# Kernel tuning notes

Hardware: AMD Instinct MI355X
Metric: run time of the kernel (lower is better)

Reference implementation:

```python
import jax, jax.numpy as jnp
import numpy as np
import math

B, NMAX, PE, E, DS, NF = 8, 128, 64, 5, 64, 8  # E = num_edge_features + 1


def setup_inputs() -> dict:
    key = jax.random.key(0)
    ks = jax.random.split(key, 10)
    total = B * NMAX
    x = jax.random.normal(ks[0], (total, PE), jnp.float32)
    batch = jnp.arange(total, dtype=jnp.int32) // NMAX  # sorted graph ids, full graphs
    q = jax.random.uniform(ks[1], (B,), jnp.float32, 0.1, 0.9)  # keep sin(2*pi*q) away from 0
    s = 0.05
    return dict(
        x=x, batch=batch, q=q,
        w_attn=jax.random.normal(ks[2], (PE, 4 * E * PE), jnp.float32) * s,
        b_attn=jnp.zeros((4 * E * PE,), jnp.float32),
        w_node=jax.random.normal(ks[3], (PE, NF), jnp.float32) * s,
        b_node=jnp.zeros((NF,), jnp.float32),
        w_phi=jax.random.normal(ks[4], (DS,), jnp.float32) * s,   # Linear(1, DS) weight
        b_phi=jax.random.normal(ks[5], (DS,), jnp.float32) * s,
        w_ctx=jax.random.normal(ks[6], (DS, DS), jnp.float32) * s,  # Linear(DS, DS, bias=False)
        w_self=jax.random.normal(ks[7], (DS,), jnp.float32) * s,  # Linear(1, DS) weight
        b_self=jax.random.normal(ks[8], (DS,), jnp.float32) * s,
        w_out=jax.random.normal(ks[9], (DS,), jnp.float32) * s,   # Linear(DS, 1) weight
        b_out=jnp.zeros((), jnp.float32),
    )


def _to_dense(batch, vals, n_graphs, n_max):
    # torch_geometric.to_dense_batch for sorted batch vector
    starts = jnp.searchsorted(batch, jnp.arange(n_graphs, dtype=batch.dtype))
    pos = jnp.arange(batch.shape[0]) - starts[batch]
    dense = jnp.zeros((n_graphs, n_max, vals.shape[-1]), vals.dtype).at[batch, pos].set(vals)
    mask = jnp.zeros((n_graphs, n_max), bool).at[batch, pos].set(True)
    return dense, mask


def reference(x, batch, q, w_attn, b_attn, w_node, b_node,
              w_phi, b_phi, w_ctx, w_self, b_self, w_out, b_out):
    scale = 1.0 / math.sqrt(E * PE)
    x_hat = x @ w_node + b_node                              # (total, NF)
    proj = x @ w_attn + b_attn                               # (total, 4*E*PE)
    dense, mask = _to_dense(batch, proj, B, NMAX)            # (B, N, 4*E*PE), (B, N)
    k1, q1, k2, q2 = jnp.split(dense, 4, axis=-1)
    heads = lambda t: t.reshape(B, NMAX, E, PE).transpose(0, 2, 1, 3)  # (B, E, N, PE)
    k1, q1, k2, q2 = heads(k1), heads(q1), heads(k2), heads(q2)
    z_re = jnp.einsum('bend,bemd->benm', k1, q1) * scale     # (B, E, N, N)
    z_im = jnp.einsum('bend,bemd->benm', k2, q2) * scale
    c = jnp.cos(2.0 * math.pi * q)[:, None, None, None]
    s = jnp.sin(2.0 * math.pi * q)[:, None, None, None]
    z = z_re + z_im * (2.0 - c) / s                          # (B, E, N, N)
    eye = jnp.eye(NMAX, dtype=bool)
    edge_mask = mask[:, :, None] & mask[:, None, :] & ~eye   # (B, N, N)
    # DeepSetClassifier
    zt = z[..., None]                                        # (B, E, N, N, 1)
    phi_out = zt * w_phi + b_phi                             # (B, E, N, N, DS)
    m = edge_mask[:, None, :, :, None].astype(z.dtype)       # (B, 1, N, N, 1)
    denom = jnp.maximum(edge_mask.sum(-1).astype(z.dtype), 1.0)[:, None, :, None]  # (B,1,N,1)
    ctx = (m * phi_out).sum(3) / denom                       # (B, E, N, DS) masked neighbor mean
    h = jax.nn.gelu(zt * w_self + b_self + (ctx @ w_ctx)[:, :, :, None, :],
                    approximate=False)                        # (B, E, N, N, DS)
    e = (h * w_out).sum(-1) + b_out                          # (B, E, N, N)
    e_hat = jnp.transpose(e, (0, 3, 2, 1))                   # transpose(-1, 1) -> (B, N, N, E)
    return (e_hat, x_hat, edge_mask, mask)
```

## Files before the change

### kernel.cpp

```cpp
#include <hip/hip_runtime.h>
#include <hip/hip_bf16.h>

#define NB 8
#define NMAXN 128
#define PEH 64
#define NE 5
#define DSZ 64
#define NFEAT 8
#define TOTALN 1024
#define PCOLS 1280

#define OUT_XHAT (NB*NMAXN*NMAXN*NE)
#define OUT_EM   (OUT_XHAT + TOTALN*NFEAT)
#define OUT_MASK (OUT_EM + NB*NMAXN*NMAXN)


__global__ void k_fused1(const float* __restrict__ x, const float* __restrict__ qv,
                         const float* __restrict__ w_attn, const float* __restrict__ b_attn,
                         const float* __restrict__ w_node, const float* __restrict__ b_node,
                         const float* __restrict__ w_phi, const float* __restrict__ b_phi,
                         const float* __restrict__ w_ctx, const float* __restrict__ b_self,
                         float* __restrict__ ws, float* __restrict__ out,
                         int offZbar, int offWpc, int offC1, int offFac, int doProj)
{
    int blk = blockIdx.x, t = threadIdx.x;
    if (blk < 256) {
        if (!doProj) return;
        __shared__ float xs[4 * 64];
        int r0 = blk * 4;
        if (t < 256) xs[t] = x[r0 * PEH + t];
        __syncthreads();
        float4 b4 = *(const float4*)&b_attn[4 * t];
        float4 a0 = b4, a1 = b4, a2 = b4, a3 = b4;
        const float* wp = w_attn + 4 * t;
        #pragma unroll 4
        for (int k = 0; k < 64; k++) {
            float4 w4 = *(const float4*)&wp[k * PCOLS];
            float x0 = xs[k], x1 = xs[64 + k], x2 = xs[128 + k], x3 = xs[192 + k];
            a0.x = fmaf(x0, w4.x, a0.x); a0.y = fmaf(x0, w4.y, a0.y); a0.z = fmaf(x0, w4.z, a0.z); a0.w = fmaf(x0, w4.w, a0.w);
            a1.x = fmaf(x1, w4.x, a1.x); a1.y = fmaf(x1, w4.y, a1.y); a1.z = fmaf(x1, w4.z, a1.z); a1.w = fmaf(x1, w4.w, a1.w);
            a2.x = fmaf(x2, w4.x, a2.x); a2.y = fmaf(x2, w4.y, a2.y); a2.z = fmaf(x2, w4.z, a2.z); a2.w = fmaf(x2, w4.w, a2.w);
            a3.x = fmaf(x3, w4.x, a3.x); a3.y = fmaf(x3, w4.y, a3.y); a3.z = fmaf(x3, w4.z, a3.z); a3.w = fmaf(x3, w4.w, a3.w);
        }
        float* pr = ws + r0 * PCOLS + 4 * t;
        *(float4*)&pr[0]         = a0;
        *(float4*)&pr[PCOLS]     = a1;
        *(float4*)&pr[2 * PCOLS] = a2;
        *(float4*)&pr[3 * PCOLS] = a3;
        return;
    }
    int b2 = blk - 256;
    if (b2 < 32) {
        if (t < 256) {
            int g = b2 * 256 + t;
            int row = g >> 3, f = g & 7;
            const float* xr = x + row * PEH;
            float acc = b_node[f];
            #pragma unroll 8
            for (int k = 0; k < PEH; k++) acc = fmaf(xr[k], w_node[k * NFEAT + f], acc);
            out[OUT_XHAT + g] = acc;
        }
    } else if (b2 < 48) {
        int base = (b2 - 32) * 8192;
        for (int g = base + t; g < base + 8192; g += 320) {
            int n = (g >> 7) & 127, m = g & 127;
            out[OUT_EM + g] = (n == m) ? 0.0f : 1.0f;
        }
    } else if (b2 == 48) {
        for (int g = t; g < 1024; g += 320) out[OUT_MASK + g] = 1.0f;
    } else if (b2 == 49) {
        if (t < 64) {
            float wpv = 0.f, bpv = 0.f;
            for (int i = 0; i < 64; i++) {
                float wc = w_ctx[i * 64 + t];
                wpv = fmaf(w_phi[i], wc, wpv);
                bpv = fmaf(b_phi[i], wc, bpv);
            }
            ws[offWpc + t] = wpv;
            ws[offC1 + t]  = b_self[t] + bpv;
        } else if (t < 72) {
            int b = t - 64;
            float qq = qv[b];
            float ang = 6.2831853071795864f * qq;
            float c = cosf(ang), s = sinf(ang);
            ws[offFac + b] = (2.0f - c) / s;
        }
    } else {
        int base = (b2 - 50) * 2560;
        for (int g = t; g < 2560; g += 320) ws[offZbar + base + g] = 0.0f;
    }
}

__global__ void k_z_fast(float* __restrict__ ws, int zsF, int offZbar, int offFac)
{
    __shared__ alignas(16) float sm[8192 + 1280 + 1024];
    float* smA = sm;
    float* smQ = sm + 8192;
    float* zp  = sm + 8192 + 1280;

    int t = threadIdx.x;
    int blk = blockIdx.x;
    int ms = blk & 7, be = blk >> 3;
    int b = be / 5, e = be - 5 * b;
    float fac = ws[offFac + b];
    const float scale = 0.05590169943749474f;
    float sfac = scale * fac;

    const float* proj = ws;
    int kn = t >> 1, kkb = (t & 1) * 32;
    int qm = t & 15, qkb = (t >> 4) * 4;

    int tx = t & 7, ty = t >> 3;
    int m0 = 2 * tx, n0 = 4 * ty;
    float acc[4][2] = {};

    for (int pass = 0; pass < 2; pass++) {
        __syncthreads();
        int colK = (pass ? 640 : 0)   + e * 64;
        int colQ = (pass ? 960 : 320) + e * 64;
        float sc = pass ? sfac : scale;
        const float* prK = proj + (b * NMAXN + kn) * PCOLS + colK + kkb;
        #pragma unroll
        for (int j4 = 0; j4 < 8; j4++) {
            float4 v = *(const float4*)&prK[4 * j4];
            smA[(kkb + 4*j4 + 0) * 128 + kn] = sc * v.x;
            smA[(kkb + 4*j4 + 1) * 128 + kn] = sc * v.y;
            smA[(kkb + 4*j4 + 2) * 128 + kn] = sc * v.z;
            smA[(kkb + 4*j4 + 3) * 128 + kn] = sc * v.w;
        }
        const float* prQ = proj + (b * NMAXN + ms * 16 + qm) * PCOLS + colQ + qkb;
        {
            float4 v = *(const float4*)&prQ[0];
            smQ[(qkb + 0) * 20 + qm] = v.x;
            smQ[(qkb + 1) * 20 + qm] = v.y;
            smQ[(qkb + 2) * 20 + qm] = v.z;
            smQ[(qkb + 3) * 20 + qm] = v.w;
        }
        __syncthreads();
        for (int k = 0; k < 64; k++) {
            float4 a4 = *(const float4*)&smA[k * 128 + n0];
            float2 q2 = *(const float2*)&smQ[k * 20 + m0];
            float ar[4] = {a4.x, a4.y, a4.z, a4.w};
            #pragma unroll
            for (int r = 0; r < 4; r++) {
                acc[r][0] = fmaf(ar[r], q2.x, acc[r][0]);
                acc[r][1] = fmaf(ar[r], q2.y, acc[r][1]);
            }
        }
    }
    __syncthreads();

    __hip_bfloat16* zsb = (__hip_bfloat16*)(ws + zsF);
    float psum[4] = {0.f, 0.f, 0.f, 0.f};
    #pragma unroll
    for (int c = 0; c < 2; c++) {
        int mg = ms * 16 + m0 + c;
        union { ushort4 u; __hip_bfloat16 h[4]; } pk;
        #pragma unroll
        for (int r = 0; r < 4; r++) {
            pk.h[r] = __float2bfloat16(acc[r][c]);
            if (mg != n0 + r) psum[r] += acc[r][c];
        }
        *(ushort4*)&zsb[((b * NMAXN + mg) * NE + e) * NMAXN + n0] = pk.u;
    }
    #pragma unroll
    for (int r = 0; r < 4; r++) zp[(n0 + r) * 8 + tx] = psum[r];
    __syncthreads();
    if (t < 128) {
        float s = 0.f;
        #pragma unroll
        for (int xx = 0; xx < 8; xx++) s += zp[t * 8 + xx];
        atomicAdd(&ws[offZbar + (b * NE + e) * NMAXN + t], s);
    }
}

__device__ __forceinline__ float gelu_fast(float x) {
    float x2 = x * x;
    float w  = -1.5957691216057308f * x * fmaf(0.044715f, x2, 1.0f);
    float ew = __expf(w);
    return x * __builtin_amdgcn_rcpf(1.0f + ew);
}

__global__ void k_epi(const float* __restrict__ ws, const float* __restrict__ w_self,
                      const float* __restrict__ w_out, const float* __restrict__ b_out,
                      float* __restrict__ out,
                      int zsF, int offZbar, int offWpc, int offC1)
{
    __shared__ alignas(16) float4 cwi[64];
    int t = threadIdx.x;
    int b = blockIdx.x >> 6, mp = blockIdx.x & 63;
    int m0 = 2 * mp;
    if (t < 64)
        cwi[t] = make_float4(w_self[t], ws[offWpc + t], ws[offC1 + t], w_out[t]);
    float zbv = ws[offZbar + b * 640 + t] * (1.0f / 127.0f);
    __syncthreads();

    const __hip_bfloat16* zsb = (const __hip_bfloat16*)(ws + zsF);
    int e = t >> 7, n = t & 127;
    float zv0 = __bfloat162float(zsb[(b * NMAXN + m0) * 640 + t]);
    float zv1 = __bfloat162float(zsb[(b * NMAXN + m0 + 1) * 640 + t]);
    float bo = b_out[0];
    float a0 = bo, a1 = bo;
    #pragma unroll 8
    for (int d = 0; d < 64; d++) {
        float4 c = cwi[d];
        float zc = fmaf(zbv, c.y, c.z);
        a0 = fmaf(gelu_fast(fmaf(zv0, c.x, zc)), c.w, a0);
        a1 = fmaf(gelu_fast(fmaf(zv1, c.x, zc)), c.w, a1);
    }
    int oo = n * NE + e;
    out[(b * NMAXN + m0) * 640 + oo]     = a0;
    out[(b * NMAXN + m0 + 1) * 640 + oo] = a1;
}

__device__ __forceinline__ void z_store4(float acc[4][4], float* ws, float* zp,
                                         int zsF, int offZbar,
                                         int b, int e, int mq, int t)
{
    int tx = t & 7, ty = t >> 3;
    int m0 = 4 * tx, n0 = 4 * ty;
    __hip_bfloat16* zsb = (__hip_bfloat16*)(ws + zsF);
    float psum[4] = {0.f, 0.f, 0.f, 0.f};
    #pragma unroll
    for (int c = 0; c < 4; c++) {
        int mg = mq * 32 + m0 + c;
        union { ushort4 u; __hip_bfloat16 h[4]; } pk;
        #pragma unroll
        for (int r = 0; r < 4; r++) {
            pk.h[r] = __float2bfloat16(acc[r][c]);
            if (mg != n0 + r) psum[r] += acc[r][c];
        }
        *(ushort4*)&zsb[((b * NMAXN + mg) * NE + e) * NMAXN + n0] = pk.u;
    }
    #pragma unroll
    for (int r = 0; r < 4; r++) zp[(n0 + r) * 8 + tx] = psum[r];
    __syncthreads();
    if (t < 128) {
        float s = 0.f;
        #pragma unroll
        for (int xx = 0; xx < 8; xx++) s += zp[t * 8 + xx];
        atomicAdd(&ws[offZbar + (b * NE + e) * NMAXN + t], s);
    }
}

__global__ void k_z_slow(const float* __restrict__ x, const float* __restrict__ w_attn,
                         const float* __restrict__ b_attn, float* __restrict__ ws,
                         int zsF, int offZbar, int offFac)
{
    __shared__ alignas(16) float sm[8320 + 2304 + 1024];
    float* xsm = sm;
    float* smA = sm;
    float* smQ = sm + 8320;
    float* zp  = sm + 8320 + 2304;

    int t = threadIdx.x;
    int blk = blockIdx.x;
    int mq = blk & 3, be = blk >> 2;
    int b = be / 5, e = be - 5 * b;
    float fac = ws[offFac + b];
    const float scale = 0.05590169943749474f;
    float sfac = scale * fac;

    int kn   = t >> 1;
    int kkb  = (t & 1) * 32;
    int qm   = t & 31;
    int qkb  = (t >> 5) * 8;
    int mglo = mq * 32 + qm;

    int tx = t & 7, ty = t >> 3;
    int m0 = 4 * tx, n0 = 4 * ty;
    float acc[4][4] = {};

    for (int pass = 0; pass < 2; pass++) {
        __syncthreads();
        for (int i = t; i < 128 * 16; i += 256) {
            int n = i >> 4, dd = (i & 15) * 4;
            float4 xv = *(const float4*)&x[(b * NMAXN + n) * PEH + dd];
            float* dst = &xsm[n * 65 + dd];
            dst[0] = xv.x; dst[1] = xv.y; dst[2] = xv.z; dst[3] = xv.w;
        }
        __syncthreads();
        int colK = (pass ? 640 : 0)   + e * 64 + kkb;
        int colQ = (pass ? 960 : 320) + e * 64 + qkb;
        float rk[32], rq[8];
        #pragma unroll
        for (int j = 0; j < 32; j++) rk[j] = b_attn[colK + j];
        #pragma unroll
        for (int j = 0; j < 8; j++)  rq[j] = b_attn[colQ + j];
        for (int d = 0; d < 64; d++) {
            const float* wrow = w_attn + d * PCOLS;
            float xk = xsm[kn * 65 + d];
            float xq = xsm[mglo * 65 + d];
            #pragma unroll
            for (int j4 = 0; j4 < 8; j4++) {
                float4 w4 = *(const float4*)&wrow[colK + 4 * j4];
                rk[4*j4+0] = fmaf(xk, w4.x, rk[4*j4+0]);
                rk[4*j4+1] = fmaf(xk, w4.y, rk[4*j4+1]);
                rk[4*j4+2] = fmaf(xk, w4.z, rk[4*j4+2]);
                rk[4*j4+3] = fmaf(xk, w4.w, rk[4*j4+3]);
            }
            #pragma unroll
            for (int j4 = 0; j4 < 2; j4++) {
                float4 w4 = *(const float4*)&wrow[colQ + 4 * j4];
                rq[4*j4+0] = fmaf(xq, w4.x, rq[4*j4+0]);
                rq[4*j4+1] = fmaf(xq, w4.y, rq[4*j4+1]);
                rq[4*j4+2] = fmaf(xq, w4.z, rq[4*j4+2]);
                rq[4*j4+3] = fmaf(xq, w4.w, rq[4*j4+3]);
            }
        }
        __syncthreads();
        float sc = pass ? sfac : scale;
        #pragma unroll
        for (int j = 0; j < 32; j++) smA[(kkb + j) * 128 + kn] = sc * rk[j];
        #pragma unroll
        for (int j = 0; j < 8; j++)  smQ[(qkb + j) * 36 + qm] = rq[j];
        __syncthreads();
        for (int k = 0; k < 64; k++) {
            float4 a4 = *(const float4*)&smA[k * 128 + n0];
            float4 q4 = *(const float4*)&smQ[k * 36 + m0];
            float ar[4] = {a4.x, a4.y, a4.z, a4.w};
            float qr[4] = {q4.x, q4.y, q4.z, q4.w};
            #pragma unroll
            for (int r = 0; r < 4; r++)
                #pragma unroll
                for (int c = 0; c < 4; c++)
                    acc[r][c] = fmaf(ar[r], qr[c], acc[r][c]);
        }
    }
    __syncthreads();
    z_store4(acc, ws, zp, zsF, offZbar, b, e, mq, t);
}

__global__ void k_epi_slow(const float* __restrict__ ws, const float* __restrict__ w_self,
                           const float* __restrict__ w_out, const float* __restrict__ b_out,
                           float* __restrict__ out,
                           int zsF, int offZbar, int offWpc, int offC1)
{
    __shared__ alignas(16) float4 cwi[64];
    int t = threadIdx.x;
    int b = blockIdx.x >> 7, m = blockIdx.x & 127;
    if (t < 64)
        cwi[t] = make_float4(w_self[t], ws[offWpc + t], ws[offC1 + t], w_out[t]);
    float zbv = ws[offZbar + b * 640 + t] * (1.0f / 127.0f);
    __syncthreads();

    const __hip_bfloat16* zsb = (const __hip_bfloat16*)(ws + zsF);
    int e = t >> 7, n = t & 127;
    float zv = __bfloat162float(zsb[(b * NMAXN + m) * 640 + t]);
    float acc = b_out[0];
    #pragma unroll 8
    for (int d = 0; d < 64; d++) {
        float4 c = cwi[d];
        float arg = fmaf(zv, c.x, fmaf(zbv, c.y, c.z));
        acc = fmaf(gelu_fast(arg), c.w, acc);
    }
    out[(b * NMAXN + m) * 640 + n * NE + e] = acc;
}

extern "C" void kernel_launch(void* const* d_in, const int* in_sizes, int n_in,
                              void* d_out, int out_size, void* d_ws, size_t ws_size,
                              hipStream_t stream)
{
    const float* x      = (const float*)d_in[0];
    const float* q      = (const float*)d_in[2];
    const float* w_attn = (const float*)d_in[3];
    const float* b_attn = (const float*)d_in[4];
    const float* w_node = (const float*)d_in[5];
    const float* b_node = (const float*)d_in[6];
    const float* w_phi  = (const float*)d_in[7];
    const float* b_phi  = (const float*)d_in[8];
    const float* w_ctx  = (const float*)d_in[9];
    const float* w_self = (const float*)d_in[10];
    const float* b_self = (const float*)d_in[11];
    const float* w_out  = (const float*)d_in[12];
    const float* b_out  = (const float*)d_in[13];
    float* ws  = (float*)d_ws;
    float* out = (float*)d_out;

    const bool big = ws_size >= (size_t)(1643656 * 4 + 64);
    const int zsF     = big ? (TOTALN * PCOLS) : 0;
    const int offZbar = zsF + 327680;
    const int offWpc  = offZbar + 5120;
    const int offC1   = offWpc + 64;
    const int offFac  = offC1 + 64;

    k_fused1<<<308, 320, 0, stream>>>(x, q, w_attn, b_attn, w_node, b_node,
                                      w_phi, b_phi, w_ctx, b_self,
                                      ws, out, offZbar, offWpc, offC1, offFac, big ? 1 : 0);
    if (big) {
        k_z_fast<<<320, 256, 0, stream>>>(ws, zsF, offZbar, offFac);
        k_epi<<<512, 640, 0, stream>>>(ws, w_self, w_out, b_out, out,
                                       zsF, offZbar, offWpc, offC1);
    } else {
        k_z_slow<<<160, 256, 0, stream>>>(x, w_attn, b_attn, ws, zsF, offZbar, offFac);
        k_epi_slow<<<1024, 640, 0, stream>>>(ws, w_self, w_out, b_out, out,
                                             zsF, offZbar, offWpc, offC1);
    }
}
```

Baseline: 119.3 us.

## Compute neighbor-mean of z algebraically from summed Q instead of atomics

Replaces the per-tile partial row sums of z with atomicAdd reduction by an algebraic form: each block sums the Q rows over all nodes, subtracts the row's own Q (the diagonal), and dots the result with K to get the masked neighbor sum directly. This removes the global atomics and the scratch reduction, and prescales by 1/127 before storing. In exchange every block redundantly reads all 128 Q rows for its graph and head from global memory, adds extra syncs, and the zero-init of zbar becomes unnecessary but still runs.

```diff
diff --git a/kernel.cpp b/kernel.cpp
--- a/kernel.cpp
+++ b/kernel.cpp
@@ -93,10 +93,10 @@
 
 __global__ void k_z_fast(float* __restrict__ ws, int zsF, int offZbar, int offFac)
 {
-    __shared__ alignas(16) float sm[8192 + 1280 + 1024];
-    float* smA = sm;
-    float* smQ = sm + 8192;
-    float* zp  = sm + 8192 + 1280;
+    __shared__ alignas(16) float smA[64 * 128];
+    __shared__ alignas(16) float smQ[64 * 20];
+    __shared__ float qpart[256];
+    __shared__ float Qs[64];
 
     int t = threadIdx.x;
     int blk = blockIdx.x;
@@ -109,10 +109,12 @@
     const float* proj = ws;
     int kn = t >> 1, kkb = (t & 1) * 32;
     int qm = t & 15, qkb = (t >> 4) * 4;
+    int qk = t & 63, qmq = t >> 6;
 
     int tx = t & 7, ty = t >> 3;
     int m0 = 2 * tx, n0 = 4 * ty;
     float acc[4][2] = {};
+    float zb_acc = 0.f;
 
     for (int pass = 0; pass < 2; pass++) {
         __syncthreads();
@@ -136,7 +138,24 @@
             smQ[(qkb + 2) * 20 + qm] = v.z;
             smQ[(qkb + 3) * 20 + qm] = v.w;
         }
-        __syncthreads();
+        {
+            const float* qcol = proj + (b * NMAXN + qmq * 32) * PCOLS + colQ + qk;
+            float s = 0.f;
+            #pragma unroll 4
+            for (int mm = 0; mm < 32; mm++) s += qcol[mm * PCOLS];
+            qpart[t] = s;
+        }
+        __syncthreads();
+        if (t < 64) Qs[t] = (qpart[t] + qpart[t + 64]) + (qpart[t + 128] + qpart[t + 192]);
+        __syncthreads();
+        if (t < 128) {
+            const float* rowq = proj + (b * NMAXN + t) * PCOLS + colQ;
+            float d = 0.f;
+            #pragma unroll 4
+            for (int k = 0; k < 64; k++)
+                d = fmaf(smA[k * 128 + t], Qs[k] - rowq[k], d);
+            zb_acc += d;
+        }
         for (int k = 0; k < 64; k++) {
             float4 a4 = *(const float4*)&smA[k * 128 + n0];
             float2 q2 = *(const float2*)&smQ[k * 20 + m0];
@@ -148,29 +167,17 @@
             }
         }
     }
-    __syncthreads();
+
+    if (t < 128) ws[offZbar + (b * NE + e) * NMAXN + t] = zb_acc * (1.0f / 127.0f);
 
     __hip_bfloat16* zsb = (__hip_bfloat16*)(ws + zsF);
-    float psum[4] = {0.f, 0.f, 0.f, 0.f};
     #pragma unroll
     for (int c = 0; c < 2; c++) {
         int mg = ms * 16 + m0 + c;
         union { ushort4 u; __hip_bfloat16 h[4]; } pk;
         #pragma unroll
-        for (int r = 0; r < 4; r++) {
-            pk.h[r] = __float2bfloat16(acc[r][c]);
-            if (mg != n0 + r) psum[r] += acc[r][c];
-        }
+        for (int r = 0; r < 4; r++) pk.h[r] = __float2bfloat16(acc[r][c]);
         *(ushort4*)&zsb[((b * NMAXN + mg) * NE + e) * NMAXN + n0] = pk.u;
-    }
-    #pragma unroll
-    for (int r = 0; r < 4; r++) zp[(n0 + r) * 8 + tx] = psum[r];
-    __syncthreads();
-    if (t < 128) {
-        float s = 0.f;
-        #pragma unroll
-        for (int xx = 0; xx < 8; xx++) s += zp[t * 8 + xx];
-        atomicAdd(&ws[offZbar + (b * NE + e) * NMAXN + t], s);
     }
 }
 
@@ -192,7 +199,7 @@
     int m0 = 2 * mp;
     if (t < 64)
         cwi[t] = make_float4(w_self[t], ws[offWpc + t], ws[offC1 + t], w_out[t]);
-    float zbv = ws[offZbar + b * 640 + t] * (1.0f / 127.0f);
+    float zbv = ws[offZbar + b * 640 + t];
     __syncthreads();
 
     const __hip_bfloat16* zsb = (const __hip_bfloat16*)(ws + zsF);
```

Result: slower. 128.7 us (+7.8%).
